# Kernel optimization log

Measured on AMD Instinct MI355X. Metric: run time of the kernel, lower is better.

## Reference

```python
import jax, jax.numpy as jnp
import numpy as np

HEADS, DH, DIM = 16, 64, 1024
GAMMA, LAMBDA_REG = 0.01, 0.001


def _ln(x, g, b, eps=1e-5):
    mu = x.mean(-1, keepdims=True)
    var = x.var(-1, keepdims=True)  # biased var, matches torch LayerNorm
    return (x - mu) / jnp.sqrt(var + eps) * g + b


def setup_inputs() -> dict:
    key = jax.random.key(0)
    ks = jax.random.split(key, 8)
    B, NQ, NK = 8, 512, 512
    inner = HEADS * DH
    rn = lambda i, shp, sc: jax.random.normal(ks[i], shp, jnp.float32) * sc
    return {
        "q": rn(0, (B, NQ, DIM), 1.0),
        "k": rn(1, (B, NK, DIM), 1.0),
        "v": rn(2, (B, NK, DIM), 1.0),
        "ln_g": jnp.ones((DIM,), jnp.float32),
        "ln_b": jnp.zeros((DIM,), jnp.float32),
        "w_in": rn(3, (DIM, inner), 0.02),
        "wp_w1": rn(4, (2 * DH, DH), 0.05),
        "wp_b1": jnp.zeros((DH,), jnp.float32),
        "wp_lng": jnp.ones((DH,), jnp.float32),
        "wp_lnb": jnp.zeros((DH,), jnp.float32),
        "wp_w2": rn(5, (DH, DH // 2), 0.05),
        "wp_b2": jnp.zeros((DH // 2,), jnp.float32),
        "wp_w3": rn(6, (DH // 2, 3), 0.05),
        "wp_b3": jnp.zeros((3,), jnp.float32),
        "w_temp": jnp.ones((1,), jnp.float32) * 0.8,
        "w_out": rn(7, (inner, DIM), 0.02),
        "b_out": jnp.zeros((DIM,), jnp.float32),
    }


def reference(q, k, v, ln_g, ln_b, w_in, wp_w1, wp_b1, wp_lng, wp_lnb,
              wp_w2, wp_b2, wp_w3, wp_b3, w_temp, w_out, b_out):
    sg = jax.lax.stop_gradient

    def proj(x):  # input_linear (dropout=identity in eval) + head split
        y = _ln(x, ln_g, ln_b) @ w_in                      # [B,N,inner]
        B, N, _ = y.shape
        return y.reshape(B, N, HEADS, DH).transpose(2, 0, 1, 3)  # [h,B,N,d]

    f_q, f_k, f_v = proj(q), proj(k), proj(v)
    m = f_k.shape[2]
    eps = 1e-8

    # --- cosine component (clamp applied twice, as in source) ---
    dots = jnp.einsum('hbnd,hbmd->hbnm', f_q, f_k)
    n1 = jnp.linalg.norm(f_q, axis=-1, keepdims=True) + eps   # [h,B,Nq,1]
    n2 = jnp.linalg.norm(f_k, axis=-1, keepdims=True) + eps   # [h,B,Nk,1]
    cosine_sim = jnp.clip(dots / (n1 * jnp.swapaxes(n2, -1, -2)), -0.98, 0.98)

    # --- regularized covariance component ---
    f_kc = f_k - f_k.mean(axis=2, keepdims=True)
    f_qc = f_q - f_q.mean(axis=-1, keepdims=True)
    cov = jnp.einsum('hbnd,hbmd->hbnm', f_qc, f_kc) / (DH ** 0.5 + 1e-6)
    health = jnp.std(cov, ddof=1)
    base = LAMBDA_REG / max(m, 1)
    reg = jnp.where(health < 1e-5, base * 5.0,
                    jnp.where(health < 1e-3, base * 2.0, base))
    cov = jnp.clip(reg * cov, -25.0, 25.0)

    # --- margin-based variance component (eval: adaptive_gamma = gamma) ---
    fqn = f_q / jnp.maximum(jnp.linalg.norm(f_q, axis=-1, keepdims=True), 1e-6)
    fkn = f_k / jnp.maximum(jnp.linalg.norm(f_k, axis=-1, keepdims=True), 1e-6)
    cs = jnp.clip(jnp.einsum('hbnd,hbmd->hbnm', fqn, fkn), -0.98, 0.98)
    margin = jnp.clip(GAMMA - cs, 0.0, 5.0)
    var_c = jnp.broadcast_to(margin.mean(-1, keepdims=True), cs.shape)

    # --- dynamic per-head weight predictor MLP ---
    qk = jnp.concatenate([f_q.mean(axis=(1, 2)), f_k.mean(axis=(1, 2))], -1)  # [h,2d]
    h1 = jax.nn.relu(_ln(qk @ wp_w1 + wp_b1, wp_lng, wp_lnb))
    h2 = jax.nn.relu(h1 @ wp_w2 + wp_b2)
    logits = jax.nn.softmax(h2 @ wp_w3 + wp_b3, -1)  # MLP ends in Softmax
    temp = jnp.clip(w_temp, 0.1, 5.0)
    w = jax.nn.softmax(logits / temp, -1)            # second softmax with temp
    w = jnp.clip(w, 0.08, 0.75)
    w = w / w.sum(-1, keepdims=True)
    cw = w[:, 0].reshape(HEADS, 1, 1, 1)
    covw = w[:, 1].reshape(HEADS, 1, 1, 1)
    varw = w[:, 2].reshape(HEADS, 1, 1, 1)

    # --- health-based normalization (stds detached, as in source) ---
    cn = sg(jnp.std(cosine_sim, ddof=1)) + 1e-6
    covn = sg(jnp.std(cov, ddof=1)) + 1e-6
    varn = sg(jnp.std(var_c, ddof=1)) + 1e-6
    ch = jnp.minimum(cn, 1.0)
    covh = jnp.minimum(covn * 10.0, 1.0)
    varh = jnp.minimum(varn * 10.0, 1.0)
    dots_f = (cw * (cosine_sim / cn * ch)
              + covw * (cov / covn * 0.4 * covh)
              + varw * (var_c / varn * 0.4 * varh))

    # --- diversity-adaptive softmax temperature ---
    div = jnp.std(dots_f, ddof=1)
    atemp = jnp.where(div < 1e-5, 0.05, jnp.where(div < 1e-3, 0.2, 0.5 + div))
    atemp = jnp.clip(atemp, 0.05, 2.0)
    attn = jax.nn.softmax(dots_f / atemp, axis=-1)

    out = jnp.einsum('hbnm,hbmd->hbnd', attn, f_v)
    out = out.transpose(1, 2, 0, 3).reshape(q.shape[0], q.shape[1], HEADS * DH)
    return out @ w_out + b_out  # output_linear (dropout=identity)
```

## Files before the change

### kernel.cpp

```cpp
#include <hip/hip_runtime.h>
#include <math.h>

#define NHEADS 16
#define DHEAD  64
#define NDIM   1024
#define NB     8
#define NSEQ   512
#define NROWS  4096
#define NHB    128
#define NTOTD  33554432.0

typedef __bf16 bf16x8 __attribute__((ext_vector_type(8)));
typedef __bf16 bf16x4 __attribute__((ext_vector_type(4)));
typedef float  f32x4  __attribute__((ext_vector_type(4)));

#define MFMA(a,b,c) __builtin_amdgcn_mfma_f32_16x16x32_bf16(a,b,c,0,0,0)

#define O_DSUMH  0
#define O_DSUME  1024
#define O_SCAL   2048
#define O_COEF   3072
#define O_W      4096
#define O_RQ1    131072
#define O_RQ2    393216
#define O_MQ     655360
#define O_QDMK   917504
#define O_RK1    1179648
#define O_RK2    1441792
#define O_KS2    1703936
#define O_MARG   1966080
#define O_RCS    2228224
#define O_RCOV   2490368
#define O_MK     2752512
#define O_QCOL   2785280
#define O_QHI    4194304
#define O_QLO    12582912
#define O_KHI    20971520
#define O_KLO    29360128
#define O_VTH    37748736
#define O_VTL    46137344
#define O_LNST   54525952
#define O_WTH    71303168
#define O_WTL    73400320
#define O_OUTH   75497472
#define O_OUTL   83886080
#define O_WOTH   92274688
#define O_WOTL   94371840

static __device__ __forceinline__ float clamp98(float x){ return fminf(fmaxf(x,-0.98f),0.98f); }

static __device__ __forceinline__ float4 ld4hl(const __bf16* __restrict__ h,
                                               const __bf16* __restrict__ l, size_t idx){
  bf16x4 hv = *(const bf16x4*)(h+idx);
  bf16x4 lv = *(const bf16x4*)(l+idx);
  return make_float4((float)hv[0]+(float)lv[0], (float)hv[1]+(float)lv[1],
                     (float)hv[2]+(float)lv[2], (float)hv[3]+(float)lv[3]);
}

__global__ __launch_bounds__(256) void ln_stats_kernel(const float* __restrict__ q,
    const float* __restrict__ k, const float* __restrict__ v, float* __restrict__ st){
  int row = blockIdx.x, t = threadIdx.x;
  const float* x = (blockIdx.y==0) ? q : (blockIdx.y==1 ? k : v);
  float4 vv = *(const float4*)(x + (size_t)row*1024 + t*4);
  float s  = vv.x+vv.y+vv.z+vv.w;
  float ss = vv.x*vv.x+vv.y*vv.y+vv.z*vv.z+vv.w*vv.w;
  for (int off=32; off; off>>=1){ s += __shfl_down(s,off); ss += __shfl_down(ss,off); }
  __shared__ float sh[8];
  if ((t&63)==0){ sh[t>>6]=s; sh[4+(t>>6)]=ss; }
  __syncthreads();
  if (t==0){
    float S=sh[0]+sh[1]+sh[2]+sh[3], SS=sh[4]+sh[5]+sh[6]+sh[7];
    float mu = S*(1.0f/1024.0f);
    st[blockIdx.y*8192 + row*2]   = mu;
    st[blockIdx.y*8192 + row*2+1] = 1.0f/sqrtf(SS*(1.0f/1024.0f) - mu*mu + 1e-5f);
  }
}

__global__ __launch_bounds__(256) void transpose_split_kernel(const float* __restrict__ wsrc,
    __bf16* __restrict__ th, __bf16* __restrict__ tl){
  __shared__ float tile[64][65];
  int k0 = blockIdx.x*64, n0 = blockIdx.y*64;
  int t = threadIdx.x;
  int c = t&63, r4 = t>>6;
  #pragma unroll
  for (int i=0;i<16;i++){
    int kr = r4 + i*4;
    tile[kr][c] = wsrc[(size_t)(k0+kr)*1024 + n0 + c];
  }
  __syncthreads();
  #pragma unroll
  for (int i=0;i<16;i++){
    int nr = r4 + i*4;
    float v = tile[c][nr];
    __bf16 hv = (__bf16)v;
    size_t o = (size_t)(n0+nr)*1024 + k0 + c;
    th[o] = hv; tl[o] = (__bf16)(v - (float)hv);
  }
}

template<int MODE>
__global__ __launch_bounds__(256) void gemm_lds_kernel(
  const float* __restrict__ X, const float* __restrict__ lnst,
  const float* __restrict__ gv, const float* __restrict__ bv,
  const __bf16* __restrict__ Ah, const __bf16* __restrict__ Al,
  const __bf16* __restrict__ Bth, const __bf16* __restrict__ Btl,
  const float* __restrict__ bias,
  __bf16* __restrict__ oh, __bf16* __restrict__ ol, float* __restrict__ of)
{
  __shared__ __bf16 Ash[128][72];
  __shared__ __bf16 Asl[128][72];
  __shared__ __bf16 Bsh[64][72];
  __shared__ __bf16 Bsl[64][72];
  int t = threadIdx.x, w = t>>6, lane = t&63, lr = lane&15, lq = lane>>4;
  int vid = blockIdx.y*16 + blockIdx.x;
  int cX = vid&7, r2 = vid>>3;
  int ytile = cX*4 + (r2>>4);
  int xtile = r2&15;
  int rbase = ytile*128;
  int cbase = xtile*64;
  int wr = w>>1, wc = w&1;
  int srow = t>>3;
  int scol = (t&7)*8;
  f32x4 acc[4][2] = {};
  for (int kt=0; kt<16; kt++){
    int k0 = kt*64;
    bf16x8 va[4], vA[4], vb[2], vB[2];
    if (MODE<2){
      float4 g0 = *(const float4*)(gv + k0 + scol);
      float4 g1 = *(const float4*)(gv + k0 + scol + 4);
      float4 b0 = *(const float4*)(bv + k0 + scol);
      float4 b1 = *(const float4*)(bv + k0 + scol + 4);
      #pragma unroll
      for (int r=0;r<4;r++){
        int row = rbase + r*32 + srow;
        size_t gi = (size_t)row*1024 + k0 + scol;
        float4 x0 = *(const float4*)(X + gi);
        float4 x1 = *(const float4*)(X + gi + 4);
        float mu = lnst[row*2], rs = lnst[row*2+1];
        float o[8];
        o[0]=(x0.x-mu)*rs*g0.x+b0.x; o[1]=(x0.y-mu)*rs*g0.y+b0.y;
        o[2]=(x0.z-mu)*rs*g0.z+b0.z; o[3]=(x0.w-mu)*rs*g0.w+b0.w;
        o[4]=(x1.x-mu)*rs*g1.x+b1.x; o[5]=(x1.y-mu)*rs*g1.y+b1.y;
        o[6]=(x1.z-mu)*rs*g1.z+b1.z; o[7]=(x1.w-mu)*rs*g1.w+b1.w;
        bf16x8 hv, lv;
        #pragma unroll
        for (int e=0;e<8;e++){
          __bf16 hb_ = (__bf16)o[e];
          hv[e] = hb_; lv[e] = (__bf16)(o[e]-(float)hb_);
        }
        va[r]=hv; vA[r]=lv;
      }
    } else {
      #pragma unroll
      for (int r=0;r<4;r++){
        size_t gi = (size_t)(rbase + r*32 + srow)*1024 + k0 + scol;
        va[r] = *(const bf16x8*)(Ah + gi);
        vA[r] = *(const bf16x8*)(Al + gi);
      }
    }
    #pragma unroll
    for (int r=0;r<2;r++){
      size_t gi = (size_t)(cbase + r*32 + srow)*1024 + k0 + scol;
      vb[r] = *(const bf16x8*)(Bth + gi);
      vB[r] = *(const bf16x8*)(Btl + gi);
    }
    #pragma unroll
    for (int r=0;r<4;r++){
      *(bf16x8*)&Ash[r*32+srow][scol] = va[r];
      *(bf16x8*)&Asl[r*32+srow][scol] = vA[r];
    }
    #pragma unroll
    for (int r=0;r<2;r++){
      *(bf16x8*)&Bsh[r*32+srow][scol] = vb[r];
      *(bf16x8*)&Bsl[r*32+srow][scol] = vB[r];
    }
    __syncthreads();
    #pragma unroll
    for (int kc=0; kc<2; kc++){
      int ko = kc*32 + lq*8;
      bf16x8 ah[4], al[4], bh[2], bl[2];
      #pragma unroll
      for (int i=0;i<4;i++){
        ah[i] = *(const bf16x8*)&Ash[wr*64 + i*16 + lr][ko];
        al[i] = *(const bf16x8*)&Asl[wr*64 + i*16 + lr][ko];
      }
      #pragma unroll
      for (int j=0;j<2;j++){
        bh[j] = *(const bf16x8*)&Bsh[wc*32 + j*16 + lr][ko];
        bl[j] = *(const bf16x8*)&Bsl[wc*32 + j*16 + lr][ko];
      }
      #pragma unroll
      for (int i=0;i<4;i++)
        #pragma unroll
        for (int j=0;j<2;j++){
          acc[i][j] = MFMA(al[i], bh[j], acc[i][j]);
          acc[i][j] = MFMA(ah[i], bl[j], acc[i][j]);
          acc[i][j] = MFMA(ah[i], bh[j], acc[i][j]);
        }
    }
    __syncthreads();
  }
  #pragma unroll
  for (int i=0;i<4;i++)
    #pragma unroll
    for (int j=0;j<2;j++)
      #pragma unroll
      for (int r=0;r<4;r++){
        int row = rbase + wr*64 + i*16 + lq*4 + r;
        int col = cbase + wc*32 + j*16 + lr;
        float v = acc[i][j][r];
        if (MODE==2){
          of[(size_t)row*1024 + col] = v + bias[col];
        } else {
          __bf16 hv = (__bf16)v;
          __bf16 lv = (__bf16)(v - (float)hv);
          size_t o;
          if (MODE==0){
            o = (size_t)(col>>6)*262144 + (size_t)row*64 + (col&63);
          } else {
            int m = row & 511, b2 = row >> 9;
            int hh = col >> 6, d = col & 63;
            int hbq = hh*8 + b2;
            o = (((size_t)hbq*4 + (d>>4))*16 + (m>>5))*512
              + (size_t)((((m>>3)&3)*16) + (d&15))*8 + (m&7);
          }
          oh[o] = hv; ol[o] = lv;
        }
      }
}

__global__ void kstats_kernel(const __bf16* __restrict__ kh, const __bf16* __restrict__ kl,
    float* __restrict__ mk, float* __restrict__ rk1, float* __restrict__ rk2, float* __restrict__ ks2){
  int hb = blockIdx.x;
  size_t base = (size_t)hb*32768;
  int t = threadIdx.x;
  int d4 = (t&15)*4, mg = t>>4;
  float4 cs = make_float4(0,0,0,0);
  for (int m=mg; m<512; m+=16){
    float4 v = ld4hl(kh, kl, base + m*64 + d4);
    cs.x+=v.x; cs.y+=v.y; cs.z+=v.z; cs.w+=v.w;
  }
  __shared__ float csum[16][64];
  __shared__ float mksum_sh;
  *(float4*)&csum[mg][d4] = cs;
  __syncthreads();
  if (t<64){
    float s=0;
    #pragma unroll
    for (int g=0;g<16;g++) s += csum[g][t];
    float v = s*(1.0f/512.0f);
    mk[hb*64+t] = v;
    csum[0][t] = v;
  }
  __syncthreads();
  if (t==0){
    float s=0;
    for (int i=0;i<64;i++) s += csum[0][i];
    mksum_sh = s;
  }
  __syncthreads();
  float mks = mksum_sh;
  int lane = t&15, rg = t>>4;
  for (int m = rg; m<512; m+=16){
    float4 v = ld4hl(kh, kl, base + m*64 + lane*4);
    float s  = v.x+v.y+v.z+v.w;
    float ss = v.x*v.x+v.y*v.y+v.z*v.z+v.w*v.w;
    for (int off=8; off; off>>=1){ s += __shfl_xor(s,off); ss += __shfl_xor(ss,off); }
    if (lane==0){
      float nk = sqrtf(ss);
      rk1[hb*512+m] = 1.0f/(nk+1e-8f);
      rk2[hb*512+m] = 1.0f/fmaxf(nk,1e-6f);
      ks2[hb*512+m] = s - mks;
    }
  }
}

__global__ void qstats_kernel(const __bf16* __restrict__ qh, const __bf16* __restrict__ ql,
    const float* __restrict__ mk, float* __restrict__ rq1, float* __restrict__ rq2,
    float* __restrict__ mq, float* __restrict__ qdotmk, float* __restrict__ qcol){
  int hb = blockIdx.x;
  size_t base = (size_t)hb*32768;
  __shared__ float mks[64];
  __shared__ float csum[16][64];
  int t = threadIdx.x;
  if (t<64) mks[t] = mk[hb*64+t];
  int d4 = (t&15)*4, mg = t>>4;
  float4 cs = make_float4(0,0,0,0);
  for (int m=mg; m<512; m+=16){
    float4 v = ld4hl(qh, ql, base + m*64 + d4);
    cs.x+=v.x; cs.y+=v.y; cs.z+=v.z; cs.w+=v.w;
  }
  *(float4*)&csum[mg][d4] = cs;
  __syncthreads();
  if (t<64){
    float s=0;
    #pragma unroll
    for (int g=0;g<16;g++) s += csum[g][t];
    qcol[hb*64+t] = s;
  }
  int lane = t&15, rg = t>>4;
  for (int n = rg; n<512; n+=16){
    float4 v  = ld4hl(qh, ql, base + n*64 + lane*4);
    float4 mv = *(float4*)&mks[lane*4];
    float s  = v.x+v.y+v.z+v.w;
    float ss = v.x*v.x+v.y*v.y+v.z*v.z+v.w*v.w;
    float qd = v.x*mv.x+v.y*mv.y+v.z*mv.z+v.w*mv.w;
    for (int off=8; off; off>>=1){ s+=__shfl_xor(s,off); ss+=__shfl_xor(ss,off); qd+=__shfl_xor(qd,off); }
    if (lane==0){
      float nq = sqrtf(ss);
      rq1[hb*512+n] = 1.0f/(nq+1e-8f);
      rq2[hb*512+n] = 1.0f/fmaxf(nq,1e-6f);
      mq[hb*512+n]  = s*(1.0f/64.0f);
      qdotmk[hb*512+n] = qd;
    }
  }
}

__global__ void mlp_kernel(const float* __restrict__ qcol, const float* __restrict__ mk,
   const float* __restrict__ w1, const float* __restrict__ b1, const float* __restrict__ lng,
   const float* __restrict__ lnb, const float* __restrict__ w2, const float* __restrict__ b2,
   const float* __restrict__ w3, const float* __restrict__ b3, const float* __restrict__ wtemp,
   float* __restrict__ W){
  int h = blockIdx.x;
  int j = threadIdx.x;
  __shared__ float qk[128], h1[64], h2[32];
  float sq=0, sk=0;
  #pragma unroll
  for (int b=0;b<8;b++){
    sq += qcol[(h*8+b)*64 + j];
    sk += mk[(h*8+b)*64 + j];
  }
  qk[j]    = sq*(1.0f/4096.0f);
  qk[64+j] = sk*(1.0f/8.0f);
  __syncthreads();
  float a = b1[j];
  for (int i=0;i<128;i++) a += qk[i]*w1[i*64+j];
  float s=a, ss=a*a;
  for (int off=32; off; off>>=1){ s += __shfl_xor(s,off); ss += __shfl_xor(ss,off); }
  float mu = s*(1.0f/64.0f), var = ss*(1.0f/64.0f)-mu*mu;
  float v = (a-mu)/sqrtf(var+1e-5f)*lng[j] + lnb[j];
  h1[j] = fmaxf(v, 0.0f);
  __syncthreads();
  if (j<32){
    float a2 = b2[j];
    for (int i=0;i<64;i++) a2 += h1[i]*w2[i*32+j];
    h2[j] = fmaxf(a2,0.0f);
  }
  __syncthreads();
  if (j==0){
    float l[3];
    for (int kq=0;kq<3;kq++){ float a3=b3[kq]; for(int i=0;i<32;i++) a3 += h2[i]*w3[i*3+kq]; l[kq]=a3; }
    float m = fmaxf(l[0],fmaxf(l[1],l[2]));
    float e0=expf(l[0]-m), e1=expf(l[1]-m), e2=expf(l[2]-m);
    float si = 1.0f/(e0+e1+e2);
    float temp = fminf(fmaxf(wtemp[0], 0.1f), 5.0f);
    float t0=e0*si/temp, t1=e1*si/temp, t2=e2*si/temp;
    float m2 = fmaxf(t0,fmaxf(t1,t2));
    float f0=expf(t0-m2), f1=expf(t1-m2), f2=expf(t2-m2);
    float s2i = 1.0f/(f0+f1+f2);
    float wv[3] = {f0*s2i, f1*s2i, f2*s2i};
    float wsum=0.0f;
    for (int kq=0;kq<3;kq++){ wv[kq]=fminf(fmaxf(wv[kq],0.08f),0.75f); wsum+=wv[kq]; }
    for (int kq=0;kq<3;kq++) W[h*3+kq] = wv[kq]/wsum;
  }
}

__global__ __launch_bounds__(256) void s1_mfma_kernel(
  const __bf16* __restrict__ qhp, const __bf16* __restrict__ qlp,
  const __bf16* __restrict__ khp, const __bf16* __restrict__ klp,
  const float* __restrict__ rq1, const float* __restrict__ rq2,
  const float* __restrict__ mq, const float* __restrict__ qdmk,
  const float* __restrict__ rk1, const float* __restrict__ rk2,
  const float* __restrict__ ks2,
  double* __restrict__ dsumH, float* __restrict__ margin,
  float* __restrict__ rcs, float* __restrict__ rcov)
{
  int vid = blockIdx.y*4 + blockIdx.x;
  int cX = vid&7, r2 = vid>>3;
  int hb = cX*16 + (r2>>2);
  int n0 = (r2&3)*128;
  const __bf16* Qh = qhp + (size_t)hb*32768;
  const __bf16* Ql = qlp + (size_t)hb*32768;
  const __bf16* Kh = khp + (size_t)hb*32768;
  const __bf16* Kl = klp + (size_t)hb*32768;
  __shared__ float sm[512][3];
  __shared__ float sn[128][4];
  int t = threadIdx.x;
  for (int mm=t; mm<512; mm+=256){
    int m = hb*512 + mm;
    sm[mm][0]=rk1[m]; sm[mm][1]=rk2[m]; sm[mm][2]=ks2[m];
  }
  if (t<128){
    int n = hb*512 + n0 + t;
    sn[t][0]=rq1[n]; sn[t][1]=rq2[n]; sn[t][2]=mq[n]; sn[t][3]=qdmk[n];
  }
  __syncthreads();
  int w = t>>6, lane = t&63, lr = lane&15, lq = lane>>4;
  int nw = w*32;
  float lcs=0,lcs2=0,lcov=0,lcov2=0,lcscov=0;
  float mrow[2][4]={}, csr[2][4]={}, cvr[2][4]={};
  for (int mc=0; mc<4; mc++){
    int m0 = mc*128;
    f32x4 acc[2][8] = {};
    #pragma unroll
    for (int kc=0; kc<2; kc++){
      int koff = kc*32 + lq*8;
      bf16x8 ah[2], al[2];
      #pragma unroll
      for (int i=0;i<2;i++){
        int ar = n0 + nw + i*16 + lr;
        ah[i] = *(const bf16x8*)(Qh + ar*64 + koff);
        al[i] = *(const bf16x8*)(Ql + ar*64 + koff);
      }
      #pragma unroll
      for (int j=0;j<8;j++){
        int br = m0 + j*16 + lr;
        bf16x8 bh = *(const bf16x8*)(Kh + br*64 + koff);
        bf16x8 bl = *(const bf16x8*)(Kl + br*64 + koff);
        #pragma unroll
        for (int i=0;i<2;i++){
          acc[i][j] = MFMA(ah[i], bh, acc[i][j]);
          acc[i][j] = MFMA(ah[i], bl, acc[i][j]);
          acc[i][j] = MFMA(al[i], bh, acc[i][j]);
        }
      }
    }
    #pragma unroll
    for (int i=0;i<2;i++){
      float nr1[4],nr2[4],nmq[4],nqd[4];
      #pragma unroll
      for (int r=0;r<4;r++){
        int nl = nw + i*16 + lq*4 + r;
        nr1[r]=sn[nl][0]; nr2[r]=sn[nl][1]; nmq[r]=sn[nl][2]; nqd[r]=sn[nl][3];
      }
      #pragma unroll
      for (int j=0;j<8;j++){
        int ml = m0 + j*16 + lr;
        float k1=sm[ml][0], k2=sm[ml][1], ksv=sm[ml][2];
        #pragma unroll
        for (int r=0;r<4;r++){
          float dv = acc[i][j][r];
          float cs = clamp98(dv*nr1[r]*k1);
          float c2 = clamp98(dv*nr2[r]*k2);
          float mg = fminf(fmaxf(0.01f-c2,0.0f),5.0f);
          float cv = dv - nqd[r] - nmq[r]*ksv;
          lcs+=cs; lcs2+=cs*cs; lcov+=cv; lcov2+=cv*cv; lcscov+=cs*cv;
          mrow[i][r]+=mg; csr[i][r]+=cs; cvr[i][r]+=cv;
        }
      }
    }
  }
  for (int off=1; off<16; off<<=1)
    #pragma unroll
    for (int i=0;i<2;i++)
      #pragma unroll
      for (int r=0;r<4;r++){
        mrow[i][r]+=__shfl_xor(mrow[i][r],off);
        csr[i][r] +=__shfl_xor(csr[i][r],off);
        cvr[i][r]+=__shfl_xor(cvr[i][r],off);
      }
  if (lr==0){
    #pragma unroll
    for (int i=0;i<2;i++)
      #pragma unroll
      for (int r=0;r<4;r++){
        int n = hb*512 + n0 + nw + i*16 + lq*4 + r;
        margin[n] = mrow[i][r]*(1.0f/512.0f);
        rcs[n]    = csr[i][r];
        rcov[n]   = cvr[i][r];
      }
  }
  for (int off=32; off; off>>=1){
    lcs+=__shfl_xor(lcs,off); lcs2+=__shfl_xor(lcs2,off);
    lcov+=__shfl_xor(lcov,off); lcov2+=__shfl_xor(lcov2,off);
    lcscov+=__shfl_xor(lcscov,off);
  }
  __shared__ double red[4][5];
  if (lane==0){ red[w][0]=lcs; red[w][1]=lcs2; red[w][2]=lcov; red[w][3]=lcov2; red[w][4]=lcscov; }
  __syncthreads();
  if (t==0){
    int h = hb>>3;
    for (int c=0;c<5;c++)
      atomicAdd(&dsumH[h*5+c], red[0][c]+red[1][c]+red[2][c]+red[3][c]);
  }
}

__global__ void margfin_kernel(const float* __restrict__ margin, double* __restrict__ dsumE){
  double s=0, ss=0;
  for (int k2=0;k2<4;k2++){
    int idx = blockIdx.x*1024 + k2*256 + threadIdx.x;
    float v = margin[idx];
    s += v; ss += (double)v*v;
  }
  for (int off=32; off; off>>=1){ s+=__shfl_down(s,off); ss+=__shfl_down(ss,off); }
  __shared__ double sh[8];
  int t = threadIdx.x;
  if ((t&63)==0){ sh[t>>6]=s; sh[4+(t>>6)]=ss; }
  __syncthreads();
  if (t==0){
    atomicAdd(dsumE+0, sh[0]+sh[1]+sh[2]+sh[3]);
    atomicAdd(dsumE+1, sh[4]+sh[5]+sh[6]+sh[7]);
  }
}

__global__ void scalars1_kernel(const double* __restrict__ dsumH, double* __restrict__ dsumE,
                                const float* __restrict__ W, float* __restrict__ coef){
  double Scs=0,Scs2=0,Scov=0,Scov2=0;
  for (int h=0;h<16;h++){
    Scs += dsumH[h*5+0]; Scs2 += dsumH[h*5+1];
    Scov += dsumH[h*5+2]; Scov2 += dsumH[h*5+3];
  }
  double N = NTOTD;
  double cn = sqrt(fmax((Scs2-Scs*Scs/N)/(N-1.0),0.0)) + 1e-6;
  double ch = fmin(cn, 1.0);
  const double covscale = 1.0/8.000001;
  double sc_ = Scov*covscale, sc2_ = Scov2*covscale*covscale;
  double health = sqrt(fmax((sc2_-sc_*sc_/N)/(N-1.0),0.0));
  double base = 0.001/512.0;
  double reg = health<1e-5 ? base*5.0 : (health<1e-3 ? base*2.0 : base);
  double covn = reg*health + 1e-6;
  double covh = fmin(covn*10.0, 1.0);
  double vs = dsumE[0]*512.0, vs2 = dsumE[1]*512.0;
  double varn = sqrt(fmax((vs2 - vs*vs/N)/(N-1.0),0.0)) + 1e-6;
  double varh = fmin(varn*10.0, 1.0);
  double sdf=0, sdf2=0;
  for (int h=0;h<16;h++){
    double cC  = (double)W[h*3+0]*ch/cn;
    double cCv = (double)W[h*3+1]*reg*covscale*0.4*covh/covn;
    double cVr = (double)W[h*3+2]*0.4*varh/varn;
    coef[h*3+0] = (float)cC;
    coef[h*3+1] = (float)cCv;
    coef[h*3+2] = (float)cVr;
    sdf  += cC*dsumH[h*5+0] + cCv*dsumH[h*5+2];
    sdf2 += cC*cC*dsumH[h*5+1] + cCv*cCv*dsumH[h*5+3] + 2.0*cC*cCv*dsumH[h*5+4];
  }
  dsumE[2] = sdf;
  dsumE[3] = sdf2;
}

__global__ void rowfold_kernel(const float* __restrict__ margin, const float* __restrict__ rcs,
                               const float* __restrict__ rcov, const float* __restrict__ coef,
                               double* __restrict__ dsumE){
  int idx = blockIdx.x*256 + threadIdx.x;
  int h = idx >> 12;
  float cC = coef[h*3+0], cCv = coef[h*3+1], cVr = coef[h*3+2];
  float vc = cVr * margin[idx];
  double s0 = 512.0*(double)vc;
  double s1 = 2.0*(double)vc*((double)cC*(double)rcs[idx] + (double)cCv*(double)rcov[idx])
            + 512.0*(double)vc*(double)vc;
  for (int off=32; off; off>>=1){ s0+=__shfl_down(s0,off); s1+=__shfl_down(s1,off); }
  __shared__ double sh[8];
  int t = threadIdx.x;
  if ((t&63)==0){ sh[t>>6]=s0; sh[4+(t>>6)]=s1; }
  __syncthreads();
  if (t==0){
    atomicAdd(dsumE+2, sh[0]+sh[1]+sh[2]+sh[3]);
    atomicAdd(dsumE+3, sh[4]+sh[5]+sh[6]+sh[7]);
  }
}

__global__ void scalars2_kernel(const double* __restrict__ dsumE, float* __restrict__ scal){
  double N = NTOTD;
  double div = sqrt(fmax((dsumE[3]-dsumE[2]*dsumE[2]/N)/(N-1.0),0.0));
  double at = div<1e-5 ? 0.05 : (div<1e-3 ? 0.2 : 0.5+div);
  at = fmin(fmax(at,0.05),2.0);
  scal[0] = (float)(1.0/at);
}

#define PSTRIDE 536
__global__ __launch_bounds__(512) void s3_mfma_kernel(
  const __bf16* __restrict__ qhp, const __bf16* __restrict__ qlp,
  const __bf16* __restrict__ khp, const __bf16* __restrict__ klp,
  const __bf16* __restrict__ vth, const __bf16* __restrict__ vtl,
  const float* __restrict__ rq1, const float* __restrict__ mq,
  const float* __restrict__ qdmk, const float* __restrict__ rk1,
  const float* __restrict__ ks2, const float* __restrict__ margin,
  const float* __restrict__ coef, const float* __restrict__ scal,
  __bf16* __restrict__ outh, __bf16* __restrict__ outl)
{
  int vid = blockIdx.y*16 + blockIdx.x;
  int cX = vid&7, r2 = vid>>3;
  int hb = cX*16 + (r2>>4);
  int n0 = (r2&15)*32;
  int h = hb>>3, b = hb&7;
  const __bf16* Qh = qhp + (size_t)hb*32768;
  const __bf16* Ql = qlp + (size_t)hb*32768;
  const __bf16* Kh = khp + (size_t)hb*32768;
  const __bf16* Kl = klp + (size_t)hb*32768;

  __shared__ unsigned short Plds[32][PSTRIDE];
  __shared__ float nst[32][4];
  __shared__ float mst[512][2];
  __shared__ float pmax[32][8];
  __shared__ float psum[32][8];

  int t = threadIdx.x, w = t>>6, lane = t&63, lr = lane&15, lq = lane>>4;
  if (t<32){
    int n = hb*512 + n0 + t;
    nst[t][0] = rq1[n]; nst[t][1] = mq[n]; nst[t][2] = qdmk[n];
    nst[t][3] = coef[h*3+2]*margin[n];
  }
  {
    int m = hb*512 + t;
    mst[t][0] = rk1[m]; mst[t][1] = ks2[m];
  }
  float cC = coef[h*3+0], cCv = coef[h*3+1];
  float invat = scal[0];
  __syncthreads();

  int ms0 = w*64;
  f32x4 acc[2][4] = {};
  #pragma unroll
  for (int kc=0; kc<2; kc++){
    int koff = kc*32 + lq*8;
    bf16x8 qhf[2], qlf[2];
    #pragma unroll
    for (int i=0;i<2;i++){
      int ai = (n0 + i*16 + lr)*64 + koff;
      qhf[i] = *(const bf16x8*)(Qh + ai);
      qlf[i] = *(const bf16x8*)(Ql + ai);
    }
    #pragma unroll
    for (int j=0;j<4;j++){
      int bi = (ms0 + j*16 + lr)*64 + koff;
      bf16x8 khf = *(const bf16x8*)(Kh + bi);
      bf16x8 klf = *(const bf16x8*)(Kl + bi);
      #pragma unroll
      for (int i=0;i<2;i++){
        acc[i][j] = MFMA(qlf[i], khf, acc[i][j]);
        acc[i][j] = MFMA(qhf[i], klf, acc[i][j]);
        acc[i][j] = MFMA(qhf[i], khf, acc[i][j]);
      }
    }
  }
  float rmax[2][4];
  #pragma unroll
  for (int i=0;i<2;i++){
    float a0[4],a1[4],a2[4],a3[4];
    #pragma unroll
    for (int r=0;r<4;r++){
      int nl = i*16 + lq*4 + r;
      a0[r]=nst[nl][0]; a1[r]=nst[nl][1]; a2[r]=nst[nl][2]; a3[r]=nst[nl][3];
      rmax[i][r] = -1e30f;
    }
    #pragma unroll
    for (int j=0;j<4;j++){
      int m = ms0 + j*16 + lr;
      float k1 = mst[m][0], ksv = mst[m][1];
      #pragma unroll
      for (int r=0;r<4;r++){
        float dv = acc[i][j][r];
        float cs = clamp98(dv*a0[r]*k1);
        float covr = dv - a2[r] - a1[r]*ksv;
        float df = cC*cs + cCv*covr + a3[r];
        acc[i][j][r] = df;
        rmax[i][r] = fmaxf(rmax[i][r], df);
      }
    }
  }
  #pragma unroll
  for (int i=0;i<2;i++)
    #pragma unroll
    for (int r=0;r<4;r++)
      for (int off=1; off<16; off<<=1)
        rmax[i][r] = fmaxf(rmax[i][r], __shfl_xor(rmax[i][r], off));
  if (lr==0){
    #pragma unroll
    for (int i=0;i<2;i++)
      #pragma unroll
      for (int r=0;r<4;r++)
        pmax[i*16+lq*4+r][w] = rmax[i][r];
  }
  __syncthreads();
  float rsum[2][4] = {};
  #pragma unroll
  for (int i=0;i<2;i++){
    float Mf[4];
    #pragma unroll
    for (int r=0;r<4;r++){
      int nl = i*16+lq*4+r;
      float m0_ = fmaxf(fmaxf(pmax[nl][0],pmax[nl][1]),fmaxf(pmax[nl][2],pmax[nl][3]));
      float m1_ = fmaxf(fmaxf(pmax[nl][4],pmax[nl][5]),fmaxf(pmax[nl][6],pmax[nl][7]));
      Mf[r] = fmaxf(m0_,m1_);
    }
    #pragma unroll
    for (int j=0;j<4;j++){
      int m = ms0 + j*16 + lr;
      #pragma unroll
      for (int r=0;r<4;r++){
        float p = __expf((acc[i][j][r]-Mf[r])*invat);
        rsum[i][r] += p;
        *(__bf16*)&Plds[i*16+lq*4+r][m] = (__bf16)p;
      }
    }
  }
  #pragma unroll
  for (int i=0;i<2;i++)
    #pragma unroll
    for (int r=0;r<4;r++)
      for (int off=1; off<16; off<<=1)
        rsum[i][r] += __shfl_xor(rsum[i][r], off);
  if (lr==0){
    #pragma unroll
    for (int i=0;i<2;i++)
      #pragma unroll
      for (int r=0;r<4;r++)
        psum[i*16+lq*4+r][w] = rsum[i][r];
  }
  __syncthreads();

  int rt = (w&1)*16;
  int dtg = w>>1;
  f32x4 acc2 = {};
  for (int kc=0; kc<16; kc++){
    bf16x8 pa = *(const bf16x8*)&Plds[rt+lr][kc*32 + lq*8];
    size_t vi = (((size_t)hb*4 + dtg)*16 + kc)*512 + (size_t)lane*8;
    bf16x8 vh = *(const bf16x8*)(vth + vi);
    bf16x8 vl = *(const bf16x8*)(vtl + vi);
    acc2 = MFMA(pa, vl, acc2);
    acc2 = MFMA(pa, vh, acc2);
  }
  float rsinv[4];
  #pragma unroll
  for (int r=0;r<4;r++){
    int nl = rt + lq*4 + r;
    float s0_ = psum[nl][0]+psum[nl][1]+psum[nl][2]+psum[nl][3];
    float s1_ = psum[nl][4]+psum[nl][5]+psum[nl][6]+psum[nl][7];
    rsinv[r] = 1.0f/(s0_+s1_);
  }
  #pragma unroll
  for (int r=0;r<4;r++){
    float o = acc2[r]*rsinv[r];
    int rowg = b*512 + n0 + rt + lq*4 + r;
    int colg = h*64 + dtg*16 + lr;
    size_t oi = (size_t)rowg*1024 + colg;
    __bf16 hv = (__bf16)o;
    outh[oi] = hv;
    outl[oi] = (__bf16)(o - (float)hv);
  }
}

extern "C" void kernel_launch(void* const* d_in, const int* in_sizes, int n_in,
                              void* d_out, int out_size, void* d_ws, size_t ws_size,
                              hipStream_t stream) {
  (void)in_sizes; (void)n_in; (void)out_size; (void)ws_size;
  const float* q     = (const float*)d_in[0];
  const float* k     = (const float*)d_in[1];
  const float* v     = (const float*)d_in[2];
  const float* ln_g  = (const float*)d_in[3];
  const float* ln_b  = (const float*)d_in[4];
  const float* w_in  = (const float*)d_in[5];
  const float* wp_w1 = (const float*)d_in[6];
  const float* wp_b1 = (const float*)d_in[7];
  const float* wp_lng= (const float*)d_in[8];
  const float* wp_lnb= (const float*)d_in[9];
  const float* wp_w2 = (const float*)d_in[10];
  const float* wp_b2 = (const float*)d_in[11];
  const float* wp_w3 = (const float*)d_in[12];
  const float* wp_b3 = (const float*)d_in[13];
  const float* w_temp= (const float*)d_in[14];
  const float* w_out = (const float*)d_in[15];
  const float* b_out = (const float*)d_in[16];

  char* ws = (char*)d_ws;
  double* dsumH = (double*)(ws + O_DSUMH);
  double* dsumE = (double*)(ws + O_DSUME);
  float* scal  = (float*)(ws + O_SCAL);
  float* coef  = (float*)(ws + O_COEF);
  float* W     = (float*)(ws + O_W);
  float* rq1   = (float*)(ws + O_RQ1);
  float* rq2   = (float*)(ws + O_RQ2);
  float* mqp   = (float*)(ws + O_MQ);
  float* qdmk  = (float*)(ws + O_QDMK);
  float* rk1   = (float*)(ws + O_RK1);
  float* rk2   = (float*)(ws + O_RK2);
  float* ks2   = (float*)(ws + O_KS2);
  float* marg  = (float*)(ws + O_MARG);
  float* rcs   = (float*)(ws + O_RCS);
  float* rcov  = (float*)(ws + O_RCOV);
  float* mk    = (float*)(ws + O_MK);
  float* qcol  = (float*)(ws + O_QCOL);
  float* lnst  = (float*)(ws + O_LNST);
  __bf16* qhi  = (__bf16*)(ws + O_QHI);
  __bf16* qlo  = (__bf16*)(ws + O_QLO);
  __bf16* khi  = (__bf16*)(ws + O_KHI);
  __bf16* klo  = (__bf16*)(ws + O_KLO);
  __bf16* vth  = (__bf16*)(ws + O_VTH);
  __bf16* vtl  = (__bf16*)(ws + O_VTL);
  __bf16* wth  = (__bf16*)(ws + O_WTH);
  __bf16* wtl  = (__bf16*)(ws + O_WTL);
  __bf16* outh = (__bf16*)(ws + O_OUTH);
  __bf16* outl = (__bf16*)(ws + O_OUTL);
  __bf16* woth = (__bf16*)(ws + O_WOTH);
  __bf16* wotl = (__bf16*)(ws + O_WOTL);
  float* outf  = (float*)d_out;

  hipMemsetAsync(ws + O_DSUMH, 0, 2048, stream);

  transpose_split_kernel<<<dim3(16,16),256,0,stream>>>(w_in,  wth, wtl);
  transpose_split_kernel<<<dim3(16,16),256,0,stream>>>(w_out, woth, wotl);
  ln_stats_kernel<<<dim3(4096,3),256,0,stream>>>(q, k, v, lnst);

  gemm_lds_kernel<0><<<dim3(16,32),256,0,stream>>>(q, lnst,        ln_g, ln_b, nullptr,nullptr, wth, wtl, nullptr, qhi, qlo, nullptr);
  gemm_lds_kernel<0><<<dim3(16,32),256,0,stream>>>(k, lnst+8192,   ln_g, ln_b, nullptr,nullptr, wth, wtl, nullptr, khi, klo, nullptr);
  gemm_lds_kernel<1><<<dim3(16,32),256,0,stream>>>(v, lnst+16384,  ln_g, ln_b, nullptr,nullptr, wth, wtl, nullptr, vth, vtl, nullptr);

  kstats_kernel<<<128,256,0,stream>>>(khi, klo, mk, rk1, rk2, ks2);
  qstats_kernel<<<128,256,0,stream>>>(qhi, qlo, mk, rq1, rq2, mqp, qdmk, qcol);
  mlp_kernel<<<16,64,0,stream>>>(qcol,mk,wp_w1,wp_b1,wp_lng,wp_lnb,wp_w2,wp_b2,wp_w3,wp_b3,w_temp,W);

  s1_mfma_kernel<<<dim3(4,128),256,0,stream>>>(qhi,qlo,khi,klo,rq1,rq2,mqp,qdmk,rk1,rk2,ks2,
                                               dsumH,marg,rcs,rcov);
  margfin_kernel<<<64,256,0,stream>>>(marg, dsumE);
  scalars1_kernel<<<1,1,0,stream>>>(dsumH, dsumE, W, coef);
  rowfold_kernel<<<256,256,0,stream>>>(marg, rcs, rcov, coef, dsumE);
  scalars2_kernel<<<1,1,0,stream>>>(dsumE, scal);

  s3_mfma_kernel<<<dim3(16,128),512,0,stream>>>(qhi,qlo,khi,klo,vth,vtl,
                                                rq1,mqp,qdmk,rk1,ks2,marg,coef,scal,outh,outl);
  gemm_lds_kernel<2><<<dim3(16,32),256,0,stream>>>(nullptr,nullptr,nullptr,nullptr, outh, outl, woth, wotl, b_out, nullptr,nullptr, outf);
}
```

Baseline: 388.1 us.

## Store Q/K in MFMA fragment layout and merge three projection GEMMs into one launch

Q and K projections are now written in a tiled layout in which each 16-row by 8-column MFMA fragment is contiguous. The attention kernels can then load a fragment with one contiguous 16-byte load per lane instead of strided row reads. The kstats and qstats kernels are rewritten to read the new layout with 8-wide vectors. The three projection GEMMs are merged into a single launch over a z dimension, which triples the grid size and removes two launches. The risk is that the scattered epilogue stores into the tiled layout become less coalesced.

```diff
diff --git a/kernel.cpp b/kernel.cpp
--- a/kernel.cpp
+++ b/kernel.cpp
@@ -15,6 +15,10 @@
 typedef float  f32x4  __attribute__((ext_vector_type(4)));
 
 #define MFMA(a,b,c) __builtin_amdgcn_mfma_f32_16x16x32_bf16(a,b,c,0,0,0)
+
+static __device__ __forceinline__ size_t qk_off(int hbq, int n, int d){
+  return ((size_t)hbq*32 + (n>>4))*1024 + (size_t)(d>>3)*128 + (size_t)(n&15)*8 + (d&7);
+}
 
 #define O_DSUMH  0
 #define O_DSUME  1024
@@ -49,14 +53,6 @@
 
 static __device__ __forceinline__ float clamp98(float x){ return fminf(fmaxf(x,-0.98f),0.98f); }
 
-static __device__ __forceinline__ float4 ld4hl(const __bf16* __restrict__ h,
-                                               const __bf16* __restrict__ l, size_t idx){
-  bf16x4 hv = *(const bf16x4*)(h+idx);
-  bf16x4 lv = *(const bf16x4*)(l+idx);
-  return make_float4((float)hv[0]+(float)lv[0], (float)hv[1]+(float)lv[1],
-                     (float)hv[2]+(float)lv[2], (float)hv[3]+(float)lv[3]);
-}
-
 __global__ __launch_bounds__(256) void ln_stats_kernel(const float* __restrict__ q,
     const float* __restrict__ k, const float* __restrict__ v, float* __restrict__ st){
   int row = blockIdx.x, t = threadIdx.x;
@@ -98,14 +94,133 @@
   }
 }
 
-template<int MODE>
-__global__ __launch_bounds__(256) void gemm_lds_kernel(
-  const float* __restrict__ X, const float* __restrict__ lnst,
+__global__ __launch_bounds__(256) void proj_gemm_kernel(
+  const float* __restrict__ q, const float* __restrict__ k, const float* __restrict__ v,
+  const float* __restrict__ lnst0,
   const float* __restrict__ gv, const float* __restrict__ bv,
+  const __bf16* __restrict__ Bth, const __bf16* __restrict__ Btl,
+  __bf16* __restrict__ qhi, __bf16* __restrict__ qlo,
+  __bf16* __restrict__ khi, __bf16* __restrict__ klo,
+  __bf16* __restrict__ vth, __bf16* __restrict__ vtl)
+{
+  __shared__ __bf16 Ash[128][72];
+  __shared__ __bf16 Asl[128][72];
+  __shared__ __bf16 Bsh[64][72];
+  __shared__ __bf16 Bsl[64][72];
+  int z = blockIdx.z;
+  const float* X = (z==0)? q : (z==1? k : v);
+  const float* lnst = lnst0 + z*8192;
+  __bf16* oh = (z==0)? qhi : (z==1? khi : vth);
+  __bf16* ol = (z==0)? qlo : (z==1? klo : vtl);
+  int t = threadIdx.x, w = t>>6, lane = t&63, lr = lane&15, lq = lane>>4;
+  int vid = blockIdx.y*16 + blockIdx.x;
+  int cX = vid&7, r2 = vid>>3;
+  int ytile = cX*4 + (r2>>4);
+  int xtile = r2&15;
+  int rbase = ytile*128;
+  int cbase = xtile*64;
+  int wr = w>>1, wc = w&1;
+  int srow = t>>3;
+  int scol = (t&7)*8;
+  f32x4 acc[4][2] = {};
+  for (int kt=0; kt<16; kt++){
+    int k0 = kt*64;
+    bf16x8 va[4], vA[4], vb[2], vB[2];
+    float4 g0 = *(const float4*)(gv + k0 + scol);
+    float4 g1 = *(const float4*)(gv + k0 + scol + 4);
+    float4 b0 = *(const float4*)(bv + k0 + scol);
+    float4 b1 = *(const float4*)(bv + k0 + scol + 4);
+    #pragma unroll
+    for (int r=0;r<4;r++){
+      int row = rbase + r*32 + srow;
+      size_t gi = (size_t)row*1024 + k0 + scol;
+      float4 x0 = *(const float4*)(X + gi);
+      float4 x1 = *(const float4*)(X + gi + 4);
+      float mu = lnst[row*2], rs = lnst[row*2+1];
+      float o[8];
+      o[0]=(x0.x-mu)*rs*g0.x+b0.x; o[1]=(x0.y-mu)*rs*g0.y+b0.y;
+      o[2]=(x0.z-mu)*rs*g0.z+b0.z; o[3]=(x0.w-mu)*rs*g0.w+b0.w;
+      o[4]=(x1.x-mu)*rs*g1.x+b1.x; o[5]=(x1.y-mu)*rs*g1.y+b1.y;
+      o[6]=(x1.z-mu)*rs*g1.z+b1.z; o[7]=(x1.w-mu)*rs*g1.w+b1.w;
+      bf16x8 hv, lv;
+      #pragma unroll
+      for (int e=0;e<8;e++){
+        __bf16 hb_ = (__bf16)o[e];
+        hv[e] = hb_; lv[e] = (__bf16)(o[e]-(float)hb_);
+      }
+      va[r]=hv; vA[r]=lv;
+    }
+    #pragma unroll
+    for (int r=0;r<2;r++){
+      size_t gi = (size_t)(cbase + r*32 + srow)*1024 + k0 + scol;
+      vb[r] = *(const bf16x8*)(Bth + gi);
+      vB[r] = *(const bf16x8*)(Btl + gi);
+    }
+    #pragma unroll
+    for (int r=0;r<4;r++){
+      *(bf16x8*)&Ash[r*32+srow][scol] = va[r];
+      *(bf16x8*)&Asl[r*32+srow][scol] = vA[r];
+    }
+    #pragma unroll
+    for (int r=0;r<2;r++){
+      *(bf16x8*)&Bsh[r*32+srow][scol] = vb[r];
+      *(bf16x8*)&Bsl[r*32+srow][scol] = vB[r];
+    }
+    __syncthreads();
+    #pragma unroll
+    for (int kc=0; kc<2; kc++){
+      int ko = kc*32 + lq*8;
+      bf16x8 ah[4], al[4], bh[2], bl[2];
+      #pragma unroll
+      for (int i=0;i<4;i++){
+        ah[i] = *(const bf16x8*)&Ash[wr*64 + i*16 + lr][ko];
+        al[i] = *(const bf16x8*)&Asl[wr*64 + i*16 + lr][ko];
+      }
+      #pragma unroll
+      for (int j=0;j<2;j++){
+        bh[j] = *(const bf16x8*)&Bsh[wc*32 + j*16 + lr][ko];
+        bl[j] = *(const bf16x8*)&Bsl[wc*32 + j*16 + lr][ko];
+      }
+      #pragma unroll
+      for (int i=0;i<4;i++)
+        #pragma unroll
+        for (int j=0;j<2;j++){
+          acc[i][j] = MFMA(al[i], bh[j], acc[i][j]);
+          acc[i][j] = MFMA(ah[i], bl[j], acc[i][j]);
+          acc[i][j] = MFMA(ah[i], bh[j], acc[i][j]);
+        }
+    }
+    __syncthreads();
+  }
+  #pragma unroll
+  for (int i=0;i<4;i++)
+    #pragma unroll
+    for (int j=0;j<2;j++)
+      #pragma unroll
+      for (int r=0;r<4;r++){
+        int row = rbase + wr*64 + i*16 + lq*4 + r;
+        int col = cbase + wc*32 + j*16 + lr;
+        float val = acc[i][j][r];
+        __bf16 hv = (__bf16)val;
+        __bf16 lv = (__bf16)(val - (float)hv);
+        int n = row & 511, b2 = row >> 9;
+        int hh = col >> 6, d = col & 63;
+        int hbq = hh*8 + b2;
+        size_t o;
+        if (z<2){
+          o = qk_off(hbq, n, d);
+        } else {
+          o = (((size_t)hbq*4 + (d>>4))*16 + (n>>5))*512
+            + (size_t)((((n>>3)&3)*16) + (d&15))*8 + (n&7);
+        }
+        oh[o] = hv; ol[o] = lv;
+      }
+}
+
+__global__ __launch_bounds__(256) void final_gemm_kernel(
   const __bf16* __restrict__ Ah, const __bf16* __restrict__ Al,
   const __bf16* __restrict__ Bth, const __bf16* __restrict__ Btl,
-  const float* __restrict__ bias,
-  __bf16* __restrict__ oh, __bf16* __restrict__ ol, float* __restrict__ of)
+  const float* __restrict__ bias, float* __restrict__ of)
 {
   __shared__ __bf16 Ash[128][72];
   __shared__ __bf16 Asl[128][72];
@@ -125,38 +240,11 @@
   for (int kt=0; kt<16; kt++){
     int k0 = kt*64;
     bf16x8 va[4], vA[4], vb[2], vB[2];
-    if (MODE<2){
-      float4 g0 = *(const float4*)(gv + k0 + scol);
-      float4 g1 = *(const float4*)(gv + k0 + scol + 4);
-      float4 b0 = *(const float4*)(bv + k0 + scol);
-      float4 b1 = *(const float4*)(bv + k0 + scol + 4);
-      #pragma unroll
-      for (int r=0;r<4;r++){
-        int row = rbase + r*32 + srow;
-        size_t gi = (size_t)row*1024 + k0 + scol;
-        float4 x0 = *(const float4*)(X + gi);
-        float4 x1 = *(const float4*)(X + gi + 4);
-        float mu = lnst[row*2], rs = lnst[row*2+1];
-        float o[8];
-        o[0]=(x0.x-mu)*rs*g0.x+b0.x; o[1]=(x0.y-mu)*rs*g0.y+b0.y;
-        o[2]=(x0.z-mu)*rs*g0.z+b0.z; o[3]=(x0.w-mu)*rs*g0.w+b0.w;
-        o[4]=(x1.x-mu)*rs*g1.x+b1.x; o[5]=(x1.y-mu)*rs*g1.y+b1.y;
-        o[6]=(x1.z-mu)*rs*g1.z+b1.z; o[7]=(x1.w-mu)*rs*g1.w+b1.w;
-        bf16x8 hv, lv;
-        #pragma unroll
-        for (int e=0;e<8;e++){
-          __bf16 hb_ = (__bf16)o[e];
-          hv[e] = hb_; lv[e] = (__bf16)(o[e]-(float)hb_);
-        }
-        va[r]=hv; vA[r]=lv;
-      }
-    } else {
-      #pragma unroll
-      for (int r=0;r<4;r++){
-        size_t gi = (size_t)(rbase + r*32 + srow)*1024 + k0 + scol;
-        va[r] = *(const bf16x8*)(Ah + gi);
-        vA[r] = *(const bf16x8*)(Al + gi);
-      }
+    #pragma unroll
+    for (int r=0;r<4;r++){
+      size_t gi = (size_t)(rbase + r*32 + srow)*1024 + k0 + scol;
+      va[r] = *(const bf16x8*)(Ah + gi);
+      vA[r] = *(const bf16x8*)(Al + gi);
     }
     #pragma unroll
     for (int r=0;r<2;r++){
@@ -208,24 +296,7 @@
       for (int r=0;r<4;r++){
         int row = rbase + wr*64 + i*16 + lq*4 + r;
         int col = cbase + wc*32 + j*16 + lr;
-        float v = acc[i][j][r];
-        if (MODE==2){
-          of[(size_t)row*1024 + col] = v + bias[col];
-        } else {
-          __bf16 hv = (__bf16)v;
-          __bf16 lv = (__bf16)(v - (float)hv);
-          size_t o;
-          if (MODE==0){
-            o = (size_t)(col>>6)*262144 + (size_t)row*64 + (col&63);
-          } else {
-            int m = row & 511, b2 = row >> 9;
-            int hh = col >> 6, d = col & 63;
-            int hbq = hh*8 + b2;
-            o = (((size_t)hbq*4 + (d>>4))*16 + (m>>5))*512
-              + (size_t)((((m>>3)&3)*16) + (d&15))*8 + (m&7);
-          }
-          oh[o] = hv; ol[o] = lv;
-        }
+        of[(size_t)row*1024 + col] = acc[i][j][r] + bias[col];
       }
 }
 
@@ -234,39 +305,47 @@
   int hb = blockIdx.x;
   size_t base = (size_t)hb*32768;
   int t = threadIdx.x;
-  int d4 = (t&15)*4, mg = t>>4;
-  float4 cs = make_float4(0,0,0,0);
-  for (int m=mg; m<512; m+=16){
-    float4 v = ld4hl(kh, kl, base + m*64 + d4);
-    cs.x+=v.x; cs.y+=v.y; cs.z+=v.z; cs.w+=v.w;
-  }
-  __shared__ float csum[16][64];
+  __shared__ float csA[32][64];
+  __shared__ float mks_lds[64];
   __shared__ float mksum_sh;
-  *(float4*)&csum[mg][d4] = cs;
+  int c2 = t&7, mg = t>>3;
+  float fs[8] = {};
+  for (int m=mg; m<512; m+=32){
+    size_t off = base + (size_t)(m>>4)*1024 + c2*128 + (size_t)(m&15)*8;
+    bf16x8 h = *(const bf16x8*)(kh+off);
+    bf16x8 l = *(const bf16x8*)(kl+off);
+    #pragma unroll
+    for (int e=0;e<8;e++) fs[e] += (float)h[e]+(float)l[e];
+  }
+  #pragma unroll
+  for (int e=0;e<8;e++) csA[mg][c2*8+e] = fs[e];
   __syncthreads();
   if (t<64){
     float s=0;
     #pragma unroll
-    for (int g=0;g<16;g++) s += csum[g][t];
-    float v = s*(1.0f/512.0f);
-    mk[hb*64+t] = v;
-    csum[0][t] = v;
+    for (int g=0;g<32;g++) s += csA[g][t];
+    float vv = s*(1.0f/512.0f);
+    mk[hb*64+t] = vv;
+    mks_lds[t] = vv;
   }
   __syncthreads();
   if (t==0){
     float s=0;
-    for (int i=0;i<64;i++) s += csum[0][i];
+    for (int i=0;i<64;i++) s += mks_lds[i];
     mksum_sh = s;
   }
   __syncthreads();
   float mks = mksum_sh;
-  int lane = t&15, rg = t>>4;
-  for (int m = rg; m<512; m+=16){
-    float4 v = ld4hl(kh, kl, base + m*64 + lane*4);
-    float s  = v.x+v.y+v.z+v.w;
-    float ss = v.x*v.x+v.y*v.y+v.z*v.z+v.w*v.w;
-    for (int off=8; off; off>>=1){ s += __shfl_xor(s,off); ss += __shfl_xor(ss,off); }
-    if (lane==0){
+  int l8 = t&7, rg = t>>3;
+  for (int m=rg; m<512; m+=32){
+    size_t off = base + (size_t)(m>>4)*1024 + l8*128 + (size_t)(m&15)*8;
+    bf16x8 h = *(const bf16x8*)(kh+off);
+    bf16x8 l = *(const bf16x8*)(kl+off);
+    float s=0, ss=0;
+    #pragma unroll
+    for (int e=0;e<8;e++){ float vv=(float)h[e]+(float)l[e]; s+=vv; ss+=vv*vv; }
+    for (int o2=4;o2;o2>>=1){ s+=__shfl_xor(s,o2); ss+=__shfl_xor(ss,o2); }
+    if (l8==0){
       float nk = sqrtf(ss);
       rk1[hb*512+m] = 1.0f/(nk+1e-8f);
       rk2[hb*512+m] = 1.0f/fmaxf(nk,1e-6f);
@@ -280,33 +359,44 @@
     float* __restrict__ mq, float* __restrict__ qdotmk, float* __restrict__ qcol){
   int hb = blockIdx.x;
   size_t base = (size_t)hb*32768;
-  __shared__ float mks[64];
-  __shared__ float csum[16][64];
   int t = threadIdx.x;
-  if (t<64) mks[t] = mk[hb*64+t];
-  int d4 = (t&15)*4, mg = t>>4;
-  float4 cs = make_float4(0,0,0,0);
-  for (int m=mg; m<512; m+=16){
-    float4 v = ld4hl(qh, ql, base + m*64 + d4);
-    cs.x+=v.x; cs.y+=v.y; cs.z+=v.z; cs.w+=v.w;
-  }
-  *(float4*)&csum[mg][d4] = cs;
+  __shared__ float csA[32][64];
+  __shared__ float mks_lds[64];
+  int c2 = t&7, mg = t>>3;
+  if (t<64) mks_lds[t] = mk[hb*64+t];
+  float fs[8] = {};
+  for (int m=mg; m<512; m+=32){
+    size_t off = base + (size_t)(m>>4)*1024 + c2*128 + (size_t)(m&15)*8;
+    bf16x8 h = *(const bf16x8*)(qh+off);
+    bf16x8 l = *(const bf16x8*)(ql+off);
+    #pragma unroll
+    for (int e=0;e<8;e++) fs[e] += (float)h[e]+(float)l[e];
+  }
+  #pragma unroll
+  for (int e=0;e<8;e++) csA[mg][c2*8+e] = fs[e];
   __syncthreads();
   if (t<64){
     float s=0;
     #pragma unroll
-    for (int g=0;g<16;g++) s += csum[g][t];
+    for (int g=0;g<32;g++) s += csA[g][t];
     qcol[hb*64+t] = s;
   }
-  int lane = t&15, rg = t>>4;
-  for (int n = rg; n<512; n+=16){
-    float4 v  = ld4hl(qh, ql, base + n*64 + lane*4);
-    float4 mv = *(float4*)&mks[lane*4];
-    float s  = v.x+v.y+v.z+v.w;
-    float ss = v.x*v.x+v.y*v.y+v.z*v.z+v.w*v.w;
-    float qd = v.x*mv.x+v.y*mv.y+v.z*mv.z+v.w*mv.w;
-    for (int off=8; off; off>>=1){ s+=__shfl_xor(s,off); ss+=__shfl_xor(ss,off); qd+=__shfl_xor(qd,off); }
-    if (lane==0){
+  int l8 = t&7, rg = t>>3;
+  float mkv[8];
+  #pragma unroll
+  for (int e=0;e<8;e++) mkv[e] = mks_lds[l8*8+e];
+  for (int n=rg; n<512; n+=32){
+    size_t off = base + (size_t)(n>>4)*1024 + l8*128 + (size_t)(n&15)*8;
+    bf16x8 h = *(const bf16x8*)(qh+off);
+    bf16x8 l = *(const bf16x8*)(ql+off);
+    float s=0, ss=0, qd=0;
+    #pragma unroll
+    for (int e=0;e<8;e++){
+      float vv=(float)h[e]+(float)l[e];
+      s+=vv; ss+=vv*vv; qd+=vv*mkv[e];
+    }
+    for (int o2=4;o2;o2>>=1){ s+=__shfl_xor(s,o2); ss+=__shfl_xor(ss,o2); qd+=__shfl_xor(qd,o2); }
+    if (l8==0){
       float nq = sqrtf(ss);
       rq1[hb*512+n] = 1.0f/(nq+1e-8f);
       rq2[hb*512+n] = 1.0f/fmaxf(nq,1e-6f);
@@ -379,10 +469,7 @@
   int cX = vid&7, r2 = vid>>3;
   int hb = cX*16 + (r2>>2);
   int n0 = (r2&3)*128;
-  const __bf16* Qh = qhp + (size_t)hb*32768;
-  const __bf16* Ql = qlp + (size_t)hb*32768;
-  const __bf16* Kh = khp + (size_t)hb*32768;
-  const __bf16* Kl = klp + (size_t)hb*32768;
+  size_t qb = (size_t)hb*32768;
   __shared__ float sm[512][3];
   __shared__ float sn[128][4];
   int t = threadIdx.x;
@@ -404,19 +491,18 @@
     f32x4 acc[2][8] = {};
     #pragma unroll
     for (int kc=0; kc<2; kc++){
-      int koff = kc*32 + lq*8;
       bf16x8 ah[2], al[2];
       #pragma unroll
       for (int i=0;i<2;i++){
-        int ar = n0 + nw + i*16 + lr;
-        ah[i] = *(const bf16x8*)(Qh + ar*64 + koff);
-        al[i] = *(const bf16x8*)(Ql + ar*64 + koff);
+        size_t off = qb + (size_t)(((n0+nw)>>4)+i)*1024 + kc*512 + (size_t)lane*8;
+        ah[i] = *(const bf16x8*)(qhp + off);
+        al[i] = *(const bf16x8*)(qlp + off);
       }
       #pragma unroll
       for (int j=0;j<8;j++){
-        int br = m0 + j*16 + lr;
-        bf16x8 bh = *(const bf16x8*)(Kh + br*64 + koff);
-        bf16x8 bl = *(const bf16x8*)(Kl + br*64 + koff);
+        size_t off = qb + (size_t)((m0>>4)+j)*1024 + kc*512 + (size_t)lane*8;
+        bf16x8 bh = *(const bf16x8*)(khp + off);
+        bf16x8 bl = *(const bf16x8*)(klp + off);
         #pragma unroll
         for (int i=0;i<2;i++){
           acc[i][j] = MFMA(ah[i], bh, acc[i][j]);
@@ -583,10 +669,7 @@
   int hb = cX*16 + (r2>>4);
   int n0 = (r2&15)*32;
   int h = hb>>3, b = hb&7;
-  const __bf16* Qh = qhp + (size_t)hb*32768;
-  const __bf16* Ql = qlp + (size_t)hb*32768;
-  const __bf16* Kh = khp + (size_t)hb*32768;
-  const __bf16* Kl = klp + (size_t)hb*32768;
+  size_t qb = (size_t)hb*32768;
 
   __shared__ unsigned short Plds[32][PSTRIDE];
   __shared__ float nst[32][4];
@@ -612,19 +695,18 @@
   f32x4 acc[2][4] = {};
   #pragma unroll
   for (int kc=0; kc<2; kc++){
-    int koff = kc*32 + lq*8;
     bf16x8 qhf[2], qlf[2];
     #pragma unroll
     for (int i=0;i<2;i++){
-      int ai = (n0 + i*16 + lr)*64 + koff;
-      qhf[i] = *(const bf16x8*)(Qh + ai);
-      qlf[i] = *(const bf16x8*)(Ql + ai);
+      size_t off = qb + (size_t)((n0>>4)+i)*1024 + kc*512 + (size_t)lane*8;
+      qhf[i] = *(const bf16x8*)(qhp + off);
+      qlf[i] = *(const bf16x8*)(qlp + off);
     }
     #pragma unroll
     for (int j=0;j<4;j++){
-      int bi = (ms0 + j*16 + lr)*64 + koff;
-      bf16x8 khf = *(const bf16x8*)(Kh + bi);
-      bf16x8 klf = *(const bf16x8*)(Kl + bi);
+      size_t off = qb + (size_t)((ms0>>4)+j)*1024 + kc*512 + (size_t)lane*8;
+      bf16x8 khf = *(const bf16x8*)(khp + off);
+      bf16x8 klf = *(const bf16x8*)(klp + off);
       #pragma unroll
       for (int i=0;i<2;i++){
         acc[i][j] = MFMA(qlf[i], khf, acc[i][j]);
@@ -801,9 +883,8 @@
   transpose_split_kernel<<<dim3(16,16),256,0,stream>>>(w_out, woth, wotl);
   ln_stats_kernel<<<dim3(4096,3),256,0,stream>>>(q, k, v, lnst);
 
-  gemm_lds_kernel<0><<<dim3(16,32),256,0,stream>>>(q, lnst,        ln_g, ln_b, nullptr,nullptr, wth, wtl, nullptr, qhi, qlo, nullptr);
-  gemm_lds_kernel<0><<<dim3(16,32),256,0,stream>>>(k, lnst+8192,   ln_g, ln_b, nullptr,nullptr, wth, wtl, nullptr, khi, klo, nullptr);
-  gemm_lds_kernel<1><<<dim3(16,32),256,0,stream>>>(v, lnst+16384,  ln_g, ln_b, nullptr,nullptr, wth, wtl, nullptr, vth, vtl, nullptr);
+  proj_gemm_kernel<<<dim3(16,32,3),256,0,stream>>>(q, k, v, lnst, ln_g, ln_b, wth, wtl,
+                                                   qhi, qlo, khi, klo, vth, vtl);
 
   kstats_kernel<<<128,256,0,stream>>>(khi, klo, mk, rk1, rk2, ks2);
   qstats_kernel<<<128,256,0,stream>>>(qhi, qlo, mk, rq1, rq2, mqp, qdmk, qcol);
@@ -818,5 +899,5 @@
 
   s3_mfma_kernel<<<dim3(16,128),512,0,stream>>>(qhi,qlo,khi,klo,vth,vtl,
                                                 rq1,mqp,qdmk,rk1,ks2,marg,coef,scal,outh,outl);
-  gemm_lds_kernel<2><<<dim3(16,32),256,0,stream>>>(nullptr,nullptr,nullptr,nullptr, outh, outl, woth, wotl, b_out, nullptr,nullptr, outf);
-}
+  final_gemm_kernel<<<dim3(16,32),256,0,stream>>>(outh, outl, woth, wotl, b_out, outf);
+}
```

Result: faster. 352.8 us (-9.1%).
